# Kernel optimization log

Hardware: AMD Instinct MI355X
Metric: run time of the kernel (lower is better)

## Reference

```python
import jax, jax.numpy as jnp
import numpy as np

EPS = 1e-6
B, T, D = 8, 4096, 512


def setup_inputs() -> dict:
    key = jax.random.key(0)
    ks = jax.random.split(key, 8)
    s = 1.0 / np.sqrt(D)
    return {
        "summarization": jax.random.normal(ks[0], (B, D), jnp.float32),
        "decoder_output": jax.random.normal(ks[1], (B, T, D), jnp.float32),
        "W_hist": jax.random.normal(ks[2], (D, D), jnp.float32) * s,
        "b_hist": jnp.zeros((D,), jnp.float32),
        "W1": jax.random.normal(ks[3], (D, D), jnp.float32) * s,
        "W2": jax.random.normal(ks[4], (D, D), jnp.float32) * s,
        "W_out": jax.random.normal(ks[5], (D, D), jnp.float32) * s,
        "b_out": jnp.zeros((D,), jnp.float32),
        "gamma": jnp.ones((D,), jnp.float32),
        "beta": jnp.zeros((D,), jnp.float32),
    }


def reference(summarization, decoder_output, W_hist, b_hist, W1, W2, W_out, b_out, gamma, beta):
    # Causal running mean: equivalent to tril-mask bmm / row-count, but O(T).
    tgt_len = decoder_output.shape[1]
    counts = jnp.arange(1, tgt_len + 1, dtype=decoder_output.dtype)[None, :, None]
    history = jnp.cumsum(decoder_output, axis=1) / counts            # [B,T,D]
    history = jnp.tanh(history @ W_hist + b_hist)                    # history_linear + tanh
    # TransformMinus: linear1(summ) - linear2(history), then linear_out + tanh
    summ_proj = (summarization @ W1)[:, None, :]                     # [B,1,D] broadcasts over T
    out = summ_proj - history @ W2
    future = jnp.tanh(out @ W_out + b_out)
    # LayerPostprocessing (eval: dropout = identity): LayerNorm(future + decoder_output)
    x = future + decoder_output
    mu = jnp.mean(x, axis=-1, keepdims=True)
    var = jnp.mean(jnp.square(x - mu), axis=-1, keepdims=True)
    return (x - mu) / jnp.sqrt(var + EPS) * gamma + beta
```

## Files before the change

### kernel.cpp

```cpp
#include <hip/hip_runtime.h>
#include <hip/hip_bf16.h>
#include <stdint.h>
#include <stddef.h>

#define DEV static __device__ __forceinline__

typedef __attribute__((ext_vector_type(8))) short short8;
typedef __attribute__((ext_vector_type(4))) float floatx4;

constexpr int Tn = 4096, Dn = 512;
constexpr int NC = 128, CTm = 32;

union U8s { uint4 u4; unsigned short us[8]; };
union U4f { float4 f4; float f[4]; };
union U4s { uint2 u2; unsigned short us[4]; };

DEV float b2f(unsigned short u) {
  union { unsigned int i; float f; } c; c.i = ((unsigned int)u) << 16; return c.f;
}
DEV unsigned short f2b(float f) {
  union { float f; unsigned int u; } c; c.f = f;
  unsigned int r = c.u + 0x7fffu + ((c.u >> 16) & 1u);
  return (unsigned short)(r >> 16);
}
DEV float fast_tanh(float x) {
  float e = __expf(2.0f * x);
  return 1.0f - 2.0f / (e + 1.0f);
}

typedef __attribute__((address_space(1))) void GVOID;
typedef __attribute__((address_space(3))) void LVOID;
DEV void async16(const unsigned short* g, unsigned short* l) {
  __builtin_amdgcn_global_load_lds((GVOID*)g, (LVOID*)l, 16, 0, 0);
}

__global__ void k_fuse1(const float* __restrict__ dec, float* __restrict__ part,
                        const float* __restrict__ Wh, const float* __restrict__ Wo,
                        const float* __restrict__ W1, const float* __restrict__ W2,
                        unsigned short* __restrict__ WhT, unsigned short* __restrict__ WoT,
                        unsigned short* __restrict__ W1b, unsigned short* __restrict__ W2b) {
  int blk = blockIdx.x;
  if (blk < 512) {
    int idx = blk * 256 + threadIdx.x;
    int d4 = idx & 127;
    int c  = (idx >> 7) & (NC - 1);
    int b  = idx >> 14;
    const float* p = dec + ((size_t)b * Tn + (size_t)c * CTm) * Dn + d4 * 4;
    float s[4] = {0,0,0,0};
#pragma unroll 4
    for (int i = 0; i < CTm; ++i) {
      U4f v; v.f4 = *(const float4*)(p + (size_t)i * Dn);
#pragma unroll
      for (int j = 0; j < 4; ++j) s[j] += v.f[j];
    }
    float* o = part + ((size_t)(b * NC + c)) * Dn + d4 * 4;
#pragma unroll
    for (int j = 0; j < 4; ++j) o[j] = s[j];
  } else {
    int wb = blk - 512;
    if (wb < 128) {
      const float* in = (wb < 64) ? Wh : Wo;
      unsigned short* out = (wb < 64) ? WhT : WoT;
      int lb = wb & 63;
      __shared__ float t[64][65];
      int n0 = (lb & 7) * 64, k0 = (lb >> 3) * 64;
#pragma unroll
      for (int l = 0; l < 16; ++l) {
        int lin = l * 256 + threadIdx.x;
        int r = lin >> 6, c = lin & 63;
        t[r][c] = in[(size_t)(k0 + r) * 512 + n0 + c];
      }
      __syncthreads();
#pragma unroll
      for (int l = 0; l < 16; ++l) {
        int lin = l * 256 + threadIdx.x;
        int r = lin >> 6, c = lin & 63;
        out[(size_t)(n0 + r) * 512 + k0 + c] = f2b(t[c][r]);
      }
    } else {
      const float* in = (wb < 160) ? W1 : W2;
      unsigned short* out = (wb < 160) ? W1b : W2b;
      int lb = (wb - 128) & 31;
      size_t base = ((size_t)lb * 256 + threadIdx.x) * 32;
#pragma unroll
      for (int l = 0; l < 8; ++l) {
        U4f v; v.f4 = *(const float4*)(in + base + l * 4);
        U4s o;
#pragma unroll
        for (int j = 0; j < 4; ++j) o.us[j] = f2b(v.f[j]);
        *(uint2*)(out + base + l * 4) = o.u2;
      }
    }
  }
}

template<int EPI>
DEV void gemmFW_core(const unsigned short* __restrict__ A,
                     const unsigned short* __restrict__ BT,
                     unsigned short* __restrict__ C,
                     const float* __restrict__ bias,
                     const float* __restrict__ spo,
                     const float* __restrict__ dec,
                     const float* __restrict__ gamma,
                     const float* __restrict__ beta,
                     float* __restrict__ out,
                     int m0) {
  __shared__ alignas(16) unsigned short sA[2][128 * 32];
  __shared__ alignas(16) unsigned short sB[2][512 * 32];
  __shared__ float lnS[128][4];
  __shared__ float lnQ[128][4];
  const int tid  = threadIdx.x;
  const int lane = tid & 63;
  const int w    = tid >> 6;
  const int wr   = w >> 2;
  const int wc   = w & 3;
  const int rs   = lane & 15;
  const int quad = lane >> 4;

  floatx4 acc[2][8];
#pragma unroll
  for (int i = 0; i < 2; ++i)
#pragma unroll
    for (int j = 0; j < 8; ++j) acc[i][j] = (floatx4){0.f, 0.f, 0.f, 0.f};

  auto STAGE = [&](int kt, int buf) {
    if (tid < 512) {
      int r = tid >> 2, c = tid & 3;
      int kc = (c ^ ((r >> 1) & 3)) * 8;
      async16(A + (size_t)(m0 + r) * 512 + kt + kc, &sA[buf][tid * 8]);
    }
#pragma unroll
    for (int l = 0; l < 2; ++l) {
      int ch = l * 1024 + tid;
      int r = ch >> 2, c = ch & 3;
      int kc = (c ^ ((r >> 1) & 3)) * 8;
      async16(BT + (size_t)r * 512 + kt + kc, &sB[buf][ch * 8]);
    }
  };

  auto COMPUTE = [&](int buf) {
    __builtin_amdgcn_s_setprio(1);
    const int co = (quad ^ ((rs >> 1) & 3)) * 8;
    short8 af0 = *(const short8*)(&sA[buf][(wr * 32 + rs) * 32 + co]);
    short8 af1 = *(const short8*)(&sA[buf][(wr * 32 + 16 + rs) * 32 + co]);
#pragma unroll
    for (int nj = 0; nj < 8; ++nj) {
      short8 bf = *(const short8*)(&sB[buf][(wc * 128 + nj * 16 + rs) * 32 + co]);
      acc[0][nj] = __builtin_amdgcn_mfma_f32_16x16x32_bf16(af0, bf, acc[0][nj], 0, 0, 0);
      acc[1][nj] = __builtin_amdgcn_mfma_f32_16x16x32_bf16(af1, bf, acc[1][nj], 0, 0, 0);
    }
    __builtin_amdgcn_s_setprio(0);
  };

  STAGE(0, 0);
  for (int t = 0; t < 15; ++t) {
    STAGE((t + 1) * 32, (t + 1) & 1);
    if (w < 8) asm volatile("s_waitcnt vmcnt(3)\n\ts_barrier" ::: "memory");
    else       asm volatile("s_waitcnt vmcnt(2)\n\ts_barrier" ::: "memory");
    COMPUTE(t & 1);
    asm volatile("s_barrier" ::: "memory");
  }
  asm volatile("s_waitcnt vmcnt(0)\n\ts_barrier" ::: "memory");
  COMPUTE(1);

  if constexpr (EPI == 0) {
#pragma unroll
    for (int nj = 0; nj < 8; ++nj) {
      const int colg = wc * 128 + nj * 16 + rs;
      float bb = bias[colg];
#pragma unroll
      for (int mi = 0; mi < 2; ++mi) {
#pragma unroll
        for (int r = 0; r < 4; ++r) {
          const int rowg = m0 + wr * 32 + mi * 16 + quad * 4 + r;
          C[(size_t)rowg * 512 + colg] = f2b(fast_tanh(acc[mi][nj][r] + bb));
        }
      }
    }
  } else {
    const int bidx = m0 >> 12;
#pragma unroll
    for (int mi = 0; mi < 2; ++mi) {
#pragma unroll
      for (int r = 0; r < 4; ++r) {
        const int lrow = wr * 32 + mi * 16 + quad * 4 + r;
        const size_t rowg = (size_t)(m0 + lrow);
        float s = 0.f, sq = 0.f;
#pragma unroll
        for (int nj = 0; nj < 8; ++nj) {
          const int colg = wc * 128 + nj * 16 + rs;
          float sp = spo[bidx * Dn + colg];
          float dv = dec[rowg * 512 + colg];
          float xf = fast_tanh(sp - acc[mi][nj][r]) + dv;
          acc[mi][nj][r] = xf;
          s += xf; sq += xf * xf;
        }
#pragma unroll
        for (int o = 8; o > 0; o >>= 1) { s += __shfl_xor(s, o, 64); sq += __shfl_xor(sq, o, 64); }
        if (rs == 0) { lnS[lrow][wc] = s; lnQ[lrow][wc] = sq; }
      }
    }
    __syncthreads();
#pragma unroll
    for (int mi = 0; mi < 2; ++mi) {
#pragma unroll
      for (int r = 0; r < 4; ++r) {
        const int lrow = wr * 32 + mi * 16 + quad * 4 + r;
        const size_t rowg = (size_t)(m0 + lrow);
        float s = 0.f, sq = 0.f;
#pragma unroll
        for (int k = 0; k < 4; ++k) { s += lnS[lrow][k]; sq += lnQ[lrow][k]; }
        float mu   = s * (1.0f / 512.0f);
        float var  = sq * (1.0f / 512.0f) - mu * mu;
        float rstd = rsqrtf(var + 1e-6f);
#pragma unroll
        for (int nj = 0; nj < 8; ++nj) {
          const int colg = wc * 128 + nj * 16 + rs;
          out[rowg * 512 + colg] = (acc[mi][nj][r] - mu) * rstd * gamma[colg] + beta[colg];
        }
      }
    }
  }
}

__global__ __launch_bounds__(1024)
void k_gemmH(const unsigned short* __restrict__ A, const unsigned short* __restrict__ BT,
             unsigned short* __restrict__ C, const float* __restrict__ bias) {
  gemmFW_core<0>(A, BT, C, bias, nullptr, nullptr, nullptr, nullptr, nullptr,
                 blockIdx.x * 128);
}

__global__ __launch_bounds__(1024)
void k_gemmFLN(const unsigned short* __restrict__ A, const unsigned short* __restrict__ BT,
               const float* __restrict__ spo, const float* __restrict__ dec,
               const float* __restrict__ gamma, const float* __restrict__ beta,
               float* __restrict__ out) {
  gemmFW_core<5>(A, BT, nullptr, nullptr, spo, dec, gamma, beta, out,
                 blockIdx.x * 128);
}

DEV void gemm64_core(const unsigned short* __restrict__ A,
                     const unsigned short* __restrict__ BT,
                     unsigned short* __restrict__ C, int m0) {
  __shared__ alignas(16) unsigned short sA[64 * 32];
  __shared__ alignas(16) unsigned short sB[512 * 32];
  const int tid  = threadIdx.x;
  const int lane = tid & 63;
  const int w    = tid >> 6;
  const int wr   = w >> 2;
  const int wc   = w & 3;
  const int rs   = lane & 15;
  const int quad = lane >> 4;

  floatx4 acc[2][8];
#pragma unroll
  for (int i = 0; i < 2; ++i)
#pragma unroll
    for (int j = 0; j < 8; ++j) acc[i][j] = (floatx4){0.f, 0.f, 0.f, 0.f};

  for (int t = 0; t < 16; ++t) {
    const int kt = t * 32;
    if (tid < 256) {
      int r = tid >> 2, c = tid & 3;
      int kc = (c ^ ((r >> 1) & 3)) * 8;
      async16(A + (size_t)(m0 + r) * 512 + kt + kc, &sA[tid * 8]);
    }
#pragma unroll
    for (int l = 0; l < 4; ++l) {
      int ch = l * 512 + tid;
      int r = ch >> 2, c = ch & 3;
      int kc = (c ^ ((r >> 1) & 3)) * 8;
      async16(BT + (size_t)r * 512 + kt + kc, &sB[ch * 8]);
    }
    asm volatile("s_waitcnt vmcnt(0)" ::: "memory");
    __syncthreads();

    const int co = (quad ^ ((rs >> 1) & 3)) * 8;
    short8 af0 = *(const short8*)(&sA[(wr * 32 + rs) * 32 + co]);
    short8 af1 = *(const short8*)(&sA[(wr * 32 + 16 + rs) * 32 + co]);
#pragma unroll
    for (int nj = 0; nj < 8; ++nj) {
      short8 bf = *(const short8*)(&sB[(wc * 128 + nj * 16 + rs) * 32 + co]);
      acc[0][nj] = __builtin_amdgcn_mfma_f32_16x16x32_bf16(af0, bf, acc[0][nj], 0, 0, 0);
      acc[1][nj] = __builtin_amdgcn_mfma_f32_16x16x32_bf16(af1, bf, acc[1][nj], 0, 0, 0);
    }
    __syncthreads();
  }

#pragma unroll
  for (int nj = 0; nj < 8; ++nj) {
    const int colg = wc * 128 + nj * 16 + rs;
#pragma unroll
    for (int mi = 0; mi < 2; ++mi) {
#pragma unroll
      for (int r = 0; r < 4; ++r) {
        const int rowg = m0 + wr * 32 + mi * 16 + quad * 4 + r;
        C[(size_t)rowg * 512 + colg] = f2b(acc[mi][nj][r]);
      }
    }
  }
}

__global__ __launch_bounds__(512, 4)
void k_wgemm2(const unsigned short* __restrict__ WoT,
              const unsigned short* __restrict__ W2b, const unsigned short* __restrict__ W1b,
              unsigned short* __restrict__ W2WoT, unsigned short* __restrict__ W1WoT,
              float* __restrict__ part) {
  int blk = blockIdx.x;
  if (blk < 16) {
    const unsigned short* BT = (blk & 8) ? W1b : W2b;
    unsigned short* Cc = (blk & 8) ? W1WoT : W2WoT;
    gemm64_core(WoT, BT, Cc, (blk & 7) * 64);
  } else {
    int idx = (blk - 16) * 512 + threadIdx.x;
    int d4 = idx & 127;
    int b  = idx >> 7;
    float* p = part + (size_t)b * NC * Dn + d4 * 4;
    float s[4] = {0, 0, 0, 0};
    for (int c0 = 0; c0 < NC; c0 += 8) {
      U4f v[8];
#pragma unroll
      for (int i = 0; i < 8; ++i) v[i].f4 = *(const float4*)(p + (size_t)(c0 + i) * Dn);
#pragma unroll
      for (int i = 0; i < 8; ++i) {
        U4f o;
#pragma unroll
        for (int j = 0; j < 4; ++j) { o.f[j] = s[j]; s[j] += v[i].f[j]; }
        *(float4*)(p + (size_t)(c0 + i) * Dn) = o.f4;
      }
    }
  }
}

__global__ void k_fuse3(const float* __restrict__ dec, const float* __restrict__ part,
                        unsigned short* __restrict__ M,
                        const float* __restrict__ summ,
                        const unsigned short* __restrict__ W1WoT,
                        const float* __restrict__ bo, float* __restrict__ spo) {
  int blk = blockIdx.x;
  if (blk < 512) {
    int idx = blk * 256 + threadIdx.x;
    int d4 = idx & 127;
    int c  = (idx >> 7) & (NC - 1);
    int b  = idx >> 14;
    size_t rbase = (size_t)b * Tn + (size_t)c * CTm;
    U4f s; s.f4 = *(const float4*)(part + ((size_t)b * NC + c) * Dn + d4 * 4);
    int t0 = c * CTm;
    const float* dp = dec + rbase * Dn + d4 * 4;
    unsigned short* mp = M + rbase * Dn + d4 * 4;
#pragma unroll 4
    for (int i = 0; i < CTm; ++i) {
      U4f v; v.f4 = *(const float4*)(dp + (size_t)i * Dn);
      float inv = 1.0f / (float)(t0 + i + 1);
      U4s o;
#pragma unroll
      for (int j = 0; j < 4; ++j) { s.f[j] += v.f[j]; o.us[j] = f2b(s.f[j] * inv); }
      *(uint2*)(mp + (size_t)i * Dn) = o.u2;
    }
  } else {
    int widx = (blk - 512) * 4 + (threadIdx.x >> 6);
    int lane = threadIdx.x & 63;
    int n = widx & 511; int b = widx >> 9;
    U8s w8; w8.u4 = *(const uint4*)(W1WoT + (size_t)n * Dn + lane * 8);
    U4f s0, s1;
    s0.f4 = *(const float4*)(summ + (size_t)b * Dn + lane * 8);
    s1.f4 = *(const float4*)(summ + (size_t)b * Dn + lane * 8 + 4);
    float acc = 0.f;
#pragma unroll
    for (int j = 0; j < 4; ++j) acc += s0.f[j] * b2f(w8.us[j]);
#pragma unroll
    for (int j = 0; j < 4; ++j) acc += s1.f[j] * b2f(w8.us[j + 4]);
#pragma unroll
    for (int o = 32; o > 0; o >>= 1) acc += __shfl_xor(acc, o, 64);
    if (lane == 0) spo[(size_t)b * Dn + n] = acc + bo[n];
  }
}

extern "C" void kernel_launch(void* const* d_in, const int* in_sizes, int n_in,
                              void* d_out, int out_size, void* d_ws, size_t ws_size,
                              hipStream_t stream) {
  (void)in_sizes; (void)n_in; (void)out_size; (void)ws_size;
  const float* summ = (const float*)d_in[0];
  const float* dec  = (const float*)d_in[1];
  const float* Wh   = (const float*)d_in[2];
  const float* bh   = (const float*)d_in[3];
  const float* W1   = (const float*)d_in[4];
  const float* W2   = (const float*)d_in[5];
  const float* Wo   = (const float*)d_in[6];
  const float* bo   = (const float*)d_in[7];
  const float* gam  = (const float*)d_in[8];
  const float* bet  = (const float*)d_in[9];
  float* out = (float*)d_out;

  char* ws = (char*)d_ws;
  unsigned short* Mbuf  = (unsigned short*)(ws);
  unsigned short* Hbuf  = (unsigned short*)(ws + 33554432);
  float*          part  = (float*)(ws + 67108864);
  float*          spo   = (float*)(ws + 69206016);
  unsigned short* WhT   = (unsigned short*)(ws + 69238784);
  unsigned short* WoT   = (unsigned short*)(ws + 69763072);
  unsigned short* W2b   = (unsigned short*)(ws + 70287360);
  unsigned short* W2WoT = (unsigned short*)(ws + 70811648);
  unsigned short* W1b   = (unsigned short*)(ws + 71335936);
  unsigned short* W1WoT = (unsigned short*)(ws + 71860224);

  k_fuse1<<<704, 256, 0, stream>>>(dec, part, Wh, Wo, W1, W2, WhT, WoT, W1b, W2b);

  k_wgemm2<<<18, 512, 0, stream>>>(WoT, W2b, W1b, W2WoT, W1WoT, part);

  k_fuse3<<<1536, 256, 0, stream>>>(dec, part, Mbuf, summ, W1WoT, bo, spo);

  k_gemmH<<<256, 1024, 0, stream>>>(Mbuf, WhT, Hbuf, bh);

  k_gemmFLN<<<256, 1024, 0, stream>>>(Hbuf, W2WoT, spo, dec, gam, bet, out);
}
```

Measured before the change: 231.5 us.

## Fuse history GEMM into output GEMM and drop intermediate H buffer and launches

Merges the two big GEMMs into one kernel: the tanh(M·Wh+b) tile is kept in registers, written chunk by chunk into shared memory as bf16 and consumed directly as the A operand of the second GEMM. This removes the global round trip of the H buffer. The prefix-sum scan is folded into the running-mean kernel, with each block summing the preceding chunk partials itself. The summarization projection is now computed in fp32 (summ·W1 then ·Wo) instead of through a bf16 W1·Wo product. Together these cut the pipeline from five launches to three, at the cost of more registers and shared memory per block and redundant partial-sum reads.

```diff
diff --git a/kernel.cpp b/kernel.cpp
--- a/kernel.cpp
+++ b/kernel.cpp
@@ -36,12 +36,15 @@
 
 __global__ void k_fuse1(const float* __restrict__ dec, float* __restrict__ part,
                         const float* __restrict__ Wh, const float* __restrict__ Wo,
-                        const float* __restrict__ W1, const float* __restrict__ W2,
+                        const float* __restrict__ W2, const float* __restrict__ W1,
+                        const float* __restrict__ summ,
                         unsigned short* __restrict__ WhT, unsigned short* __restrict__ WoT,
-                        unsigned short* __restrict__ W1b, unsigned short* __restrict__ W2b) {
+                        unsigned short* __restrict__ W2b, float* __restrict__ s1) {
+  __shared__ float t[64][65];
   int blk = blockIdx.x;
+  int tid = threadIdx.x;
   if (blk < 512) {
-    int idx = blk * 256 + threadIdx.x;
+    int idx = blk * 256 + tid;
     int d4 = idx & 127;
     int c  = (idx >> 7) & (NC - 1);
     int b  = idx >> 14;
@@ -56,187 +59,56 @@
     float* o = part + ((size_t)(b * NC + c)) * Dn + d4 * 4;
 #pragma unroll
     for (int j = 0; j < 4; ++j) o[j] = s[j];
+  } else if (blk < 640) {
+    int wb = blk - 512;
+    const float* in = (wb < 64) ? Wh : Wo;
+    unsigned short* out = (wb < 64) ? WhT : WoT;
+    int lb = wb & 63;
+    int n0 = (lb & 7) * 64, k0 = (lb >> 3) * 64;
+#pragma unroll
+    for (int l = 0; l < 16; ++l) {
+      int lin = l * 256 + tid;
+      int r = lin >> 6, c = lin & 63;
+      t[r][c] = in[(size_t)(k0 + r) * 512 + n0 + c];
+    }
+    __syncthreads();
+#pragma unroll
+    for (int l = 0; l < 16; ++l) {
+      int lin = l * 256 + tid;
+      int r = lin >> 6, c = lin & 63;
+      out[(size_t)(n0 + r) * 512 + k0 + c] = f2b(t[c][r]);
+    }
+  } else if (blk < 672) {
+    int lb = (blk - 640) & 31;
+    size_t base = ((size_t)lb * 256 + tid) * 32;
+#pragma unroll
+    for (int l = 0; l < 8; ++l) {
+      U4f v; v.f4 = *(const float4*)(W2 + base + l * 4);
+      U4s o;
+#pragma unroll
+      for (int j = 0; j < 4; ++j) o.us[j] = f2b(v.f[j]);
+      *(uint2*)(W2b + base + l * 4) = o.u2;
+    }
   } else {
-    int wb = blk - 512;
-    if (wb < 128) {
-      const float* in = (wb < 64) ? Wh : Wo;
-      unsigned short* out = (wb < 64) ? WhT : WoT;
-      int lb = wb & 63;
-      __shared__ float t[64][65];
-      int n0 = (lb & 7) * 64, k0 = (lb >> 3) * 64;
-#pragma unroll
-      for (int l = 0; l < 16; ++l) {
-        int lin = l * 256 + threadIdx.x;
-        int r = lin >> 6, c = lin & 63;
-        t[r][c] = in[(size_t)(k0 + r) * 512 + n0 + c];
-      }
-      __syncthreads();
-#pragma unroll
-      for (int l = 0; l < 16; ++l) {
-        int lin = l * 256 + threadIdx.x;
-        int r = lin >> 6, c = lin & 63;
-        out[(size_t)(n0 + r) * 512 + k0 + c] = f2b(t[c][r]);
-      }
-    } else {
-      const float* in = (wb < 160) ? W1 : W2;
-      unsigned short* out = (wb < 160) ? W1b : W2b;
-      int lb = (wb - 128) & 31;
-      size_t base = ((size_t)lb * 256 + threadIdx.x) * 32;
-#pragma unroll
-      for (int l = 0; l < 8; ++l) {
-        U4f v; v.f4 = *(const float4*)(in + base + l * 4);
-        U4s o;
-#pragma unroll
-        for (int j = 0; j < 4; ++j) o.us[j] = f2b(v.f[j]);
-        *(uint2*)(out + base + l * 4) = o.u2;
-      }
-    }
-  }
-}
-
-template<int EPI>
-DEV void gemmFW_core(const unsigned short* __restrict__ A,
-                     const unsigned short* __restrict__ BT,
-                     unsigned short* __restrict__ C,
-                     const float* __restrict__ bias,
-                     const float* __restrict__ spo,
-                     const float* __restrict__ dec,
-                     const float* __restrict__ gamma,
-                     const float* __restrict__ beta,
-                     float* __restrict__ out,
-                     int m0) {
-  __shared__ alignas(16) unsigned short sA[2][128 * 32];
-  __shared__ alignas(16) unsigned short sB[2][512 * 32];
-  __shared__ float lnS[128][4];
-  __shared__ float lnQ[128][4];
-  const int tid  = threadIdx.x;
-  const int lane = tid & 63;
-  const int w    = tid >> 6;
-  const int wr   = w >> 2;
-  const int wc   = w & 3;
-  const int rs   = lane & 15;
-  const int quad = lane >> 4;
-
-  floatx4 acc[2][8];
-#pragma unroll
-  for (int i = 0; i < 2; ++i)
-#pragma unroll
-    for (int j = 0; j < 8; ++j) acc[i][j] = (floatx4){0.f, 0.f, 0.f, 0.f};
-
-  auto STAGE = [&](int kt, int buf) {
-    if (tid < 512) {
-      int r = tid >> 2, c = tid & 3;
-      int kc = (c ^ ((r >> 1) & 3)) * 8;
-      async16(A + (size_t)(m0 + r) * 512 + kt + kc, &sA[buf][tid * 8]);
-    }
-#pragma unroll
-    for (int l = 0; l < 2; ++l) {
-      int ch = l * 1024 + tid;
-      int r = ch >> 2, c = ch & 3;
-      int kc = (c ^ ((r >> 1) & 3)) * 8;
-      async16(BT + (size_t)r * 512 + kt + kc, &sB[buf][ch * 8]);
-    }
-  };
-
-  auto COMPUTE = [&](int buf) {
-    __builtin_amdgcn_s_setprio(1);
-    const int co = (quad ^ ((rs >> 1) & 3)) * 8;
-    short8 af0 = *(const short8*)(&sA[buf][(wr * 32 + rs) * 32 + co]);
-    short8 af1 = *(const short8*)(&sA[buf][(wr * 32 + 16 + rs) * 32 + co]);
-#pragma unroll
-    for (int nj = 0; nj < 8; ++nj) {
-      short8 bf = *(const short8*)(&sB[buf][(wc * 128 + nj * 16 + rs) * 32 + co]);
-      acc[0][nj] = __builtin_amdgcn_mfma_f32_16x16x32_bf16(af0, bf, acc[0][nj], 0, 0, 0);
-      acc[1][nj] = __builtin_amdgcn_mfma_f32_16x16x32_bf16(af1, bf, acc[1][nj], 0, 0, 0);
-    }
-    __builtin_amdgcn_s_setprio(0);
-  };
-
-  STAGE(0, 0);
-  for (int t = 0; t < 15; ++t) {
-    STAGE((t + 1) * 32, (t + 1) & 1);
-    if (w < 8) asm volatile("s_waitcnt vmcnt(3)\n\ts_barrier" ::: "memory");
-    else       asm volatile("s_waitcnt vmcnt(2)\n\ts_barrier" ::: "memory");
-    COMPUTE(t & 1);
-    asm volatile("s_barrier" ::: "memory");
-  }
-  asm volatile("s_waitcnt vmcnt(0)\n\ts_barrier" ::: "memory");
-  COMPUTE(1);
-
-  if constexpr (EPI == 0) {
-#pragma unroll
-    for (int nj = 0; nj < 8; ++nj) {
-      const int colg = wc * 128 + nj * 16 + rs;
-      float bb = bias[colg];
-#pragma unroll
-      for (int mi = 0; mi < 2; ++mi) {
-#pragma unroll
-        for (int r = 0; r < 4; ++r) {
-          const int rowg = m0 + wr * 32 + mi * 16 + quad * 4 + r;
-          C[(size_t)rowg * 512 + colg] = f2b(fast_tanh(acc[mi][nj][r] + bb));
-        }
-      }
-    }
-  } else {
-    const int bidx = m0 >> 12;
-#pragma unroll
-    for (int mi = 0; mi < 2; ++mi) {
-#pragma unroll
-      for (int r = 0; r < 4; ++r) {
-        const int lrow = wr * 32 + mi * 16 + quad * 4 + r;
-        const size_t rowg = (size_t)(m0 + lrow);
-        float s = 0.f, sq = 0.f;
-#pragma unroll
-        for (int nj = 0; nj < 8; ++nj) {
-          const int colg = wc * 128 + nj * 16 + rs;
-          float sp = spo[bidx * Dn + colg];
-          float dv = dec[rowg * 512 + colg];
-          float xf = fast_tanh(sp - acc[mi][nj][r]) + dv;
-          acc[mi][nj][r] = xf;
-          s += xf; sq += xf * xf;
-        }
-#pragma unroll
-        for (int o = 8; o > 0; o >>= 1) { s += __shfl_xor(s, o, 64); sq += __shfl_xor(sq, o, 64); }
-        if (rs == 0) { lnS[lrow][wc] = s; lnQ[lrow][wc] = sq; }
-      }
-    }
+    int bb = blk - 672;
+    int tn = tid & 63, tj = tid >> 6;
+    float a[8] = {0,0,0,0,0,0,0,0};
+    for (int j = tj * 128; j < tj * 128 + 128; ++j) {
+      float wv = W1[(size_t)j * 512 + bb * 64 + tn];
+#pragma unroll
+      for (int b = 0; b < 8; ++b) a[b] += summ[b * 512 + j] * wv;
+    }
+    float* red = &t[0][0];
+#pragma unroll
+    for (int b = 0; b < 8; ++b) red[tj * 512 + b * 64 + tn] = a[b];
     __syncthreads();
-#pragma unroll
-    for (int mi = 0; mi < 2; ++mi) {
-#pragma unroll
-      for (int r = 0; r < 4; ++r) {
-        const int lrow = wr * 32 + mi * 16 + quad * 4 + r;
-        const size_t rowg = (size_t)(m0 + lrow);
-        float s = 0.f, sq = 0.f;
-#pragma unroll
-        for (int k = 0; k < 4; ++k) { s += lnS[lrow][k]; sq += lnQ[lrow][k]; }
-        float mu   = s * (1.0f / 512.0f);
-        float var  = sq * (1.0f / 512.0f) - mu * mu;
-        float rstd = rsqrtf(var + 1e-6f);
-#pragma unroll
-        for (int nj = 0; nj < 8; ++nj) {
-          const int colg = wc * 128 + nj * 16 + rs;
-          out[rowg * 512 + colg] = (acc[mi][nj][r] - mu) * rstd * gamma[colg] + beta[colg];
-        }
-      }
-    }
-  }
-}
-
-__global__ __launch_bounds__(1024)
-void k_gemmH(const unsigned short* __restrict__ A, const unsigned short* __restrict__ BT,
-             unsigned short* __restrict__ C, const float* __restrict__ bias) {
-  gemmFW_core<0>(A, BT, C, bias, nullptr, nullptr, nullptr, nullptr, nullptr,
-                 blockIdx.x * 128);
-}
-
-__global__ __launch_bounds__(1024)
-void k_gemmFLN(const unsigned short* __restrict__ A, const unsigned short* __restrict__ BT,
-               const float* __restrict__ spo, const float* __restrict__ dec,
-               const float* __restrict__ gamma, const float* __restrict__ beta,
-               float* __restrict__ out) {
-  gemmFW_core<5>(A, BT, nullptr, nullptr, spo, dec, gamma, beta, out,
-                 blockIdx.x * 128);
+    if (tj == 0) {
+#pragma unroll
+      for (int b = 0; b < 8; ++b)
+        s1[b * 512 + bb * 64 + tn] = red[b * 64 + tn] + red[512 + b * 64 + tn] +
+                                     red[1024 + b * 64 + tn] + red[1536 + b * 64 + tn];
+    }
+  }
 }
 
 DEV void gemm64_core(const unsigned short* __restrict__ A,
@@ -301,50 +173,62 @@
   }
 }
 
-__global__ __launch_bounds__(512, 4)
-void k_wgemm2(const unsigned short* __restrict__ WoT,
-              const unsigned short* __restrict__ W2b, const unsigned short* __restrict__ W1b,
-              unsigned short* __restrict__ W2WoT, unsigned short* __restrict__ W1WoT,
-              float* __restrict__ part) {
+__global__ __launch_bounds__(512, 2)
+void k_fuse2(const unsigned short* __restrict__ WoT, const unsigned short* __restrict__ W2b,
+             unsigned short* __restrict__ W2WoT,
+             const float* __restrict__ s1, const float* __restrict__ Wo,
+             const float* __restrict__ bo, float* __restrict__ spo,
+             const float* __restrict__ dec, const float* __restrict__ part,
+             unsigned short* __restrict__ M) {
+  __shared__ float red[8][8][64];
   int blk = blockIdx.x;
-  if (blk < 16) {
-    const unsigned short* BT = (blk & 8) ? W1b : W2b;
-    unsigned short* Cc = (blk & 8) ? W1WoT : W2WoT;
-    gemm64_core(WoT, BT, Cc, (blk & 7) * 64);
+  int tid = threadIdx.x;
+  if (blk < 8) {
+    gemm64_core(WoT, W2b, W2WoT, blk * 64);
+  } else if (blk < 16) {
+    int bb = blk - 8;
+    int tn = tid & 63, tj = tid >> 6;
+    float a[8] = {0,0,0,0,0,0,0,0};
+    for (int j = tj * 64; j < tj * 64 + 64; ++j) {
+      float wv = Wo[(size_t)j * 512 + bb * 64 + tn];
+#pragma unroll
+      for (int b = 0; b < 8; ++b) a[b] += s1[b * 512 + j] * wv;
+    }
+#pragma unroll
+    for (int b = 0; b < 8; ++b) red[tj][b][tn] = a[b];
+    __syncthreads();
+    if (tj == 0) {
+#pragma unroll
+      for (int b = 0; b < 8; ++b) {
+        float s = 0.f;
+#pragma unroll
+        for (int k = 0; k < 8; ++k) s += red[k][b][tn];
+        spo[b * 512 + bb * 64 + tn] = s + bo[bb * 64 + tn];
+      }
+    }
   } else {
-    int idx = (blk - 16) * 512 + threadIdx.x;
-    int d4 = idx & 127;
-    int b  = idx >> 7;
-    float* p = part + (size_t)b * NC * Dn + d4 * 4;
-    float s[4] = {0, 0, 0, 0};
-    for (int c0 = 0; c0 < NC; c0 += 8) {
-      U4f v[8];
-#pragma unroll
-      for (int i = 0; i < 8; ++i) v[i].f4 = *(const float4*)(p + (size_t)(c0 + i) * Dn);
-#pragma unroll
-      for (int i = 0; i < 8; ++i) {
-        U4f o;
-#pragma unroll
-        for (int j = 0; j < 4; ++j) { o.f[j] = s[j]; s[j] += v[i].f[j]; }
-        *(float4*)(p + (size_t)(c0 + i) * Dn) = o.f4;
-      }
-    }
-  }
-}
-
-__global__ void k_fuse3(const float* __restrict__ dec, const float* __restrict__ part,
-                        unsigned short* __restrict__ M,
-                        const float* __restrict__ summ,
-                        const unsigned short* __restrict__ W1WoT,
-                        const float* __restrict__ bo, float* __restrict__ spo) {
-  int blk = blockIdx.x;
-  if (blk < 512) {
-    int idx = blk * 256 + threadIdx.x;
+    int idx = (blk - 16) * 512 + tid;
     int d4 = idx & 127;
     int c  = (idx >> 7) & (NC - 1);
     int b  = idx >> 14;
     size_t rbase = (size_t)b * Tn + (size_t)c * CTm;
-    U4f s; s.f4 = *(const float4*)(part + ((size_t)b * NC + c) * Dn + d4 * 4);
+    const float* pb = part + (size_t)b * NC * Dn + d4 * 4;
+    float s[4] = {0, 0, 0, 0};
+    int cc = 0;
+    for (; cc + 8 <= c; cc += 8) {
+      U4f v[8];
+#pragma unroll
+      for (int i = 0; i < 8; ++i) v[i].f4 = *(const float4*)(pb + (size_t)(cc + i) * Dn);
+#pragma unroll
+      for (int i = 0; i < 8; ++i)
+#pragma unroll
+        for (int j = 0; j < 4; ++j) s[j] += v[i].f[j];
+    }
+    for (; cc < c; ++cc) {
+      U4f v; v.f4 = *(const float4*)(pb + (size_t)cc * Dn);
+#pragma unroll
+      for (int j = 0; j < 4; ++j) s[j] += v.f[j];
+    }
     int t0 = c * CTm;
     const float* dp = dec + rbase * Dn + d4 * 4;
     unsigned short* mp = M + rbase * Dn + d4 * 4;
@@ -354,25 +238,184 @@
       float inv = 1.0f / (float)(t0 + i + 1);
       U4s o;
 #pragma unroll
-      for (int j = 0; j < 4; ++j) { s.f[j] += v.f[j]; o.us[j] = f2b(s.f[j] * inv); }
+      for (int j = 0; j < 4; ++j) { s[j] += v.f[j]; o.us[j] = f2b(s[j] * inv); }
       *(uint2*)(mp + (size_t)i * Dn) = o.u2;
     }
-  } else {
-    int widx = (blk - 512) * 4 + (threadIdx.x >> 6);
-    int lane = threadIdx.x & 63;
-    int n = widx & 511; int b = widx >> 9;
-    U8s w8; w8.u4 = *(const uint4*)(W1WoT + (size_t)n * Dn + lane * 8);
-    U4f s0, s1;
-    s0.f4 = *(const float4*)(summ + (size_t)b * Dn + lane * 8);
-    s1.f4 = *(const float4*)(summ + (size_t)b * Dn + lane * 8 + 4);
-    float acc = 0.f;
-#pragma unroll
-    for (int j = 0; j < 4; ++j) acc += s0.f[j] * b2f(w8.us[j]);
-#pragma unroll
-    for (int j = 0; j < 4; ++j) acc += s1.f[j] * b2f(w8.us[j + 4]);
-#pragma unroll
-    for (int o = 32; o > 0; o >>= 1) acc += __shfl_xor(acc, o, 64);
-    if (lane == 0) spo[(size_t)b * Dn + n] = acc + bo[n];
+  }
+}
+
+__global__ __launch_bounds__(1024)
+void k_fused(const unsigned short* __restrict__ A,
+             const unsigned short* __restrict__ B1T,
+             const unsigned short* __restrict__ B2T,
+             const float* __restrict__ bh, const float* __restrict__ spo,
+             const float* __restrict__ dec,
+             const float* __restrict__ gamma, const float* __restrict__ beta,
+             float* __restrict__ out) {
+  __shared__ alignas(16) unsigned short sA[2][128 * 32];
+  __shared__ alignas(16) unsigned short sB[2][512 * 32];
+  __shared__ alignas(16) unsigned short sH[2][128 * 32];
+  __shared__ float lnS[128][4];
+  __shared__ float lnQ[128][4];
+  const int m0   = blockIdx.x * 128;
+  const int tid  = threadIdx.x;
+  const int lane = tid & 63;
+  const int w    = tid >> 6;
+  const int wr   = w >> 2;
+  const int wc   = w & 3;
+  const int rs   = lane & 15;
+  const int quad = lane >> 4;
+
+  floatx4 acc1[2][8], acc2[2][8];
+#pragma unroll
+  for (int i = 0; i < 2; ++i)
+#pragma unroll
+    for (int j = 0; j < 8; ++j) {
+      acc1[i][j] = (floatx4){0.f, 0.f, 0.f, 0.f};
+      acc2[i][j] = (floatx4){0.f, 0.f, 0.f, 0.f};
+    }
+
+  const int co = (quad ^ ((rs >> 1) & 3)) * 8;
+
+  auto STAGE1 = [&](int kt, int buf) {
+    if (tid < 512) {
+      int r = tid >> 2, c = tid & 3;
+      int kc = (c ^ ((r >> 1) & 3)) * 8;
+      async16(A + (size_t)(m0 + r) * 512 + kt + kc, &sA[buf][tid * 8]);
+    }
+#pragma unroll
+    for (int l = 0; l < 2; ++l) {
+      int ch = l * 1024 + tid;
+      int r = ch >> 2, c = ch & 3;
+      int kc = (c ^ ((r >> 1) & 3)) * 8;
+      async16(B1T + (size_t)r * 512 + kt + kc, &sB[buf][ch * 8]);
+    }
+  };
+  auto STAGE2 = [&](int kt, int buf) {
+#pragma unroll
+    for (int l = 0; l < 2; ++l) {
+      int ch = l * 1024 + tid;
+      int r = ch >> 2, c = ch & 3;
+      int kc = (c ^ ((r >> 1) & 3)) * 8;
+      async16(B2T + (size_t)r * 512 + kt + kc, &sB[buf][ch * 8]);
+    }
+  };
+  auto COMPUTE1 = [&](int buf) {
+    __builtin_amdgcn_s_setprio(1);
+    short8 af0 = *(const short8*)(&sA[buf][(wr * 32 + rs) * 32 + co]);
+    short8 af1 = *(const short8*)(&sA[buf][(wr * 32 + 16 + rs) * 32 + co]);
+#pragma unroll
+    for (int nj = 0; nj < 8; ++nj) {
+      short8 bf = *(const short8*)(&sB[buf][(wc * 128 + nj * 16 + rs) * 32 + co]);
+      acc1[0][nj] = __builtin_amdgcn_mfma_f32_16x16x32_bf16(af0, bf, acc1[0][nj], 0, 0, 0);
+      acc1[1][nj] = __builtin_amdgcn_mfma_f32_16x16x32_bf16(af1, bf, acc1[1][nj], 0, 0, 0);
+    }
+    __builtin_amdgcn_s_setprio(0);
+  };
+  auto COMPUTE2 = [&](int buf) {
+    __builtin_amdgcn_s_setprio(1);
+    short8 af0 = *(const short8*)(&sH[buf][(wr * 32 + rs) * 32 + co]);
+    short8 af1 = *(const short8*)(&sH[buf][(wr * 32 + 16 + rs) * 32 + co]);
+#pragma unroll
+    for (int nj = 0; nj < 8; ++nj) {
+      short8 bf = *(const short8*)(&sB[buf][(wc * 128 + nj * 16 + rs) * 32 + co]);
+      acc2[0][nj] = __builtin_amdgcn_mfma_f32_16x16x32_bf16(af0, bf, acc2[0][nj], 0, 0, 0);
+      acc2[1][nj] = __builtin_amdgcn_mfma_f32_16x16x32_bf16(af1, bf, acc2[1][nj], 0, 0, 0);
+    }
+    __builtin_amdgcn_s_setprio(0);
+  };
+
+  STAGE1(0, 0);
+  for (int t = 0; t < 15; ++t) {
+    STAGE1((t + 1) * 32, (t + 1) & 1);
+    if (w < 8) asm volatile("s_waitcnt vmcnt(3)\n\ts_barrier" ::: "memory");
+    else       asm volatile("s_waitcnt vmcnt(2)\n\ts_barrier" ::: "memory");
+    COMPUTE1(t & 1);
+    asm volatile("s_barrier" ::: "memory");
+  }
+  asm volatile("s_waitcnt vmcnt(0)\n\ts_barrier" ::: "memory");
+  COMPUTE1(1);
+
+  float bb[8];
+#pragma unroll
+  for (int nj = 0; nj < 8; ++nj) bb[nj] = bh[wc * 128 + nj * 16 + rs];
+
+  auto WRITEH = [&](int kk, int buf) {
+    if (wc == (kk >> 2)) {
+      const int njb = (kk & 3) * 2;
+#pragma unroll
+      for (int q = 0; q < 2; ++q) {
+        const int col = q * 16 + rs;
+#pragma unroll
+        for (int mi = 0; mi < 2; ++mi)
+#pragma unroll
+          for (int r = 0; r < 4; ++r) {
+            const int row = wr * 32 + mi * 16 + quad * 4 + r;
+            const int ch = (col >> 3) ^ ((row >> 1) & 3);
+            sH[buf][row * 32 + ch * 8 + (col & 7)] =
+                f2b(fast_tanh(acc1[mi][njb + q][r] + bb[njb + q]));
+          }
+      }
+    }
+  };
+
+  asm volatile("s_barrier" ::: "memory");
+
+  WRITEH(0, 0);
+  STAGE2(0, 0);
+  for (int kk = 0; kk < 16; ++kk) {
+    if (kk < 15) {
+      WRITEH(kk + 1, (kk + 1) & 1);
+      STAGE2((kk + 1) * 32, (kk + 1) & 1);
+      asm volatile("s_waitcnt vmcnt(2) lgkmcnt(0)\n\ts_barrier" ::: "memory");
+    } else {
+      asm volatile("s_waitcnt vmcnt(0) lgkmcnt(0)\n\ts_barrier" ::: "memory");
+    }
+    COMPUTE2(kk & 1);
+    asm volatile("s_barrier" ::: "memory");
+  }
+
+  const int bidx = m0 >> 12;
+#pragma unroll
+  for (int mi = 0; mi < 2; ++mi) {
+#pragma unroll
+    for (int r = 0; r < 4; ++r) {
+      const int lrow = wr * 32 + mi * 16 + quad * 4 + r;
+      const size_t rowg = (size_t)(m0 + lrow);
+      float s = 0.f, sq = 0.f;
+#pragma unroll
+      for (int nj = 0; nj < 8; ++nj) {
+        const int colg = wc * 128 + nj * 16 + rs;
+        float sp = spo[bidx * Dn + colg];
+        float dv = dec[rowg * 512 + colg];
+        float xf = fast_tanh(sp - acc2[mi][nj][r]) + dv;
+        acc2[mi][nj][r] = xf;
+        s += xf; sq += xf * xf;
+      }
+#pragma unroll
+      for (int o = 8; o > 0; o >>= 1) { s += __shfl_xor(s, o, 64); sq += __shfl_xor(sq, o, 64); }
+      if (rs == 0) { lnS[lrow][wc] = s; lnQ[lrow][wc] = sq; }
+    }
+  }
+  __syncthreads();
+#pragma unroll
+  for (int mi = 0; mi < 2; ++mi) {
+#pragma unroll
+    for (int r = 0; r < 4; ++r) {
+      const int lrow = wr * 32 + mi * 16 + quad * 4 + r;
+      const size_t rowg = (size_t)(m0 + lrow);
+      float s = 0.f, sq = 0.f;
+#pragma unroll
+      for (int k = 0; k < 4; ++k) { s += lnS[lrow][k]; sq += lnQ[lrow][k]; }
+      float mu   = s * (1.0f / 512.0f);
+      float var  = sq * (1.0f / 512.0f) - mu * mu;
+      float rstd = rsqrtf(var + 1e-6f);
+#pragma unroll
+      for (int nj = 0; nj < 8; ++nj) {
+        const int colg = wc * 128 + nj * 16 + rs;
+        out[rowg * 512 + colg] = (acc2[mi][nj][r] - mu) * rstd * gamma[colg] + beta[colg];
+      }
+    }
   }
 }
 
@@ -394,23 +437,17 @@
 
   char* ws = (char*)d_ws;
   unsigned short* Mbuf  = (unsigned short*)(ws);
-  unsigned short* Hbuf  = (unsigned short*)(ws + 33554432);
   float*          part  = (float*)(ws + 67108864);
   float*          spo   = (float*)(ws + 69206016);
   unsigned short* WhT   = (unsigned short*)(ws + 69238784);
   unsigned short* WoT   = (unsigned short*)(ws + 69763072);
   unsigned short* W2b   = (unsigned short*)(ws + 70287360);
   unsigned short* W2WoT = (unsigned short*)(ws + 70811648);
-  unsigned short* W1b   = (unsigned short*)(ws + 71335936);
-  unsigned short* W1WoT = (unsigned short*)(ws + 71860224);
-
-  k_fuse1<<<704, 256, 0, stream>>>(dec, part, Wh, Wo, W1, W2, WhT, WoT, W1b, W2b);
-
-  k_wgemm2<<<18, 512, 0, stream>>>(WoT, W2b, W1b, W2WoT, W1WoT, part);
-
-  k_fuse3<<<1536, 256, 0, stream>>>(dec, part, Mbuf, summ, W1WoT, bo, spo);
-
-  k_gemmH<<<256, 1024, 0, stream>>>(Mbuf, WhT, Hbuf, bh);
-
-  k_gemmFLN<<<256, 1024, 0, stream>>>(Hbuf, W2WoT, spo, dec, gam, bet, out);
-}
+  float*          s1    = (float*)(ws + 71335936);
+
+  k_fuse1<<<680, 256, 0, stream>>>(dec, part, Wh, Wo, W2, W1, summ, WhT, WoT, W2b, s1);
+
+  k_fuse2<<<272, 512, 0, stream>>>(WoT, W2b, W2WoT, s1, Wo, bo, spo, dec, part, Mbuf);
+
+  k_fused<<<256, 1024, 0, stream>>>(Mbuf, WhT, W2WoT, bh, spo, dec, gam, bet, out);
+}
```

After: 290.8 us. 1.26x slower.
